# Kernel tuning notes

Measured on AMD Instinct MI355X. Metric: run time of the kernel, lower is better.

The kernel has to match this reference:

```python
import jax, jax.numpy as jnp
import numpy as np

# ---- SLAYER neuron / simulation params (network.yaml equivalents) ----
THETA = 10.0       # spiking threshold
TAU_SR = 10.0      # synaptic (PSP) alpha-kernel time constant
TAU_REF = 1.0      # refractory alpha-kernel time constant
SCALE_REF = 2.0
TS = 1.0           # simulation step
T_SAMPLE = 350     # number of timesteps

B, NIN, NHID, NOUT = 32, 2312, 512, 10


def _alpha_kernel(tau, mult=1.0, eps=0.01):
    # mirrors slayer._calculateAlphaKernel truncation rule
    ks = []
    for t in np.arange(0.0, T_SAMPLE, TS):
        v = mult * t / tau * np.exp(1.0 - t / tau)
        if abs(v) < eps and t > tau:
            break
        ks.append(v)
    return jnp.asarray(np.asarray(ks, dtype=np.float32))

SRM_KERNEL = _alpha_kernel(TAU_SR)                        # truncated PSP kernel
D_REF = float(np.exp(-TS / TAU_REF))                      # geometric decay of refractory alpha kernel
C_REF = float(-SCALE_REF * THETA * np.e * TS / TAU_REF)   # refKernel[j] = C_REF * j * D_REF**j


def psp(x):
    # causal temporal conv with the SRM alpha kernel, scaled by Ts. x: (B, C, T)
    b, c, t = x.shape
    k = SRM_KERNEL.shape[0]
    out = jax.lax.conv_general_dilated(
        x.reshape(b * c, 1, t), SRM_KERNEL[::-1].reshape(1, 1, k),
        window_strides=(1,), padding=[(k - 1, 0)])
    return (out * TS).reshape(b, c, t)


def spike(u_psp):
    # Sequential thresholding with FULL refractory recurrence: a spike at time s
    # adds refKernel[n-s] = C_REF*(n-s)*D_REF**(n-s) to all future potentials.
    # The alpha kernel is realized EXACTLY by a 2-state linear recurrence (x, y):
    #   x[n] = sum_s spk[s] * d^(n-s),  y[n] = sum_s spk[s] * (n-s) * d^(n-s)
    def step(carry, p_t):
        x, y = carry
        y = D_REF * (y + x)
        u = p_t + C_REF * y           # membrane potential after refractory response
        spk = (u >= THETA).astype(p_t.dtype)
        x = D_REF * x + spk
        return (x, y), spk / TS       # SLAYER emits spikes of magnitude 1/Ts
    b, c, _ = u_psp.shape
    init = (jnp.zeros((b, c), u_psp.dtype), jnp.zeros((b, c), u_psp.dtype))
    _, s = jax.lax.scan(step, init, jnp.moveaxis(u_psp, -1, 0))
    return jnp.moveaxis(s, 0, -1)


def setup_inputs() -> dict:
    key = jax.random.key(0)
    k1, k2, k3 = jax.random.split(key, 3)
    spikeInput = (jax.random.uniform(k1, (B, NIN, T_SAMPLE)) < 0.03).astype(jnp.float32) / TS
    W1 = jax.random.normal(k2, (NHID, NIN), jnp.float32) * 0.05
    W2 = jax.random.normal(k3, (NOUT, NHID), jnp.float32) * 0.5
    return {"spikeInput": spikeInput, "W1": W1, "W2": W2}


def reference(spikeInput, W1, W2):
    # fc (1x1x1 conv == per-timestep matmul) -> psp -> spike, twice
    s1 = spike(psp(jnp.einsum('oi,bit->bot', W1, spikeInput)))
    s2 = spike(psp(jnp.einsum('oi,bit->bot', W2, s1)))
    return s2
```

## Files before the change

kernel.cpp:

```cpp
#include <hip/hip_runtime.h>
#include <hip/hip_bf16.h>
#include <math.h>

#define B_    32
#define NIN_  2312
#define NHID_ 512
#define NOUT_ 10
#define T_    350
#define KLEN  77
#define MW    40
#define NIB   37
#define NTB   6
#define MAXA2 320

__global__ __launch_bounds__(256) void w1t_k(const float* __restrict__ W,
                                             float* __restrict__ WT) {
  __shared__ float tile[32][33];
  int i0 = blockIdx.x * 32, o0 = blockIdx.y * 32;
  int tx = threadIdx.x, tyb = threadIdx.y;
#pragma unroll
  for (int s = 0; s < 4; ++s) {
    int ty = tyb + s * 8;
    int o = o0 + ty, i = i0 + tx;
    if (i < NIN_) tile[ty][tx] = W[(size_t)o * NIN_ + i];
  }
  __syncthreads();
#pragma unroll
  for (int s = 0; s < 4; ++s) {
    int ty = tyb + s * 8;
    int i = i0 + ty, o = o0 + tx;
    if (i < NIN_) WT[(size_t)i * NHID_ + o] = tile[tx][ty];
  }
}

__global__ __launch_bounds__(256) void inmask_k(const float* __restrict__ X,
                                                unsigned long long* __restrict__ msk) {
  __shared__ unsigned short bits[64][4];
  int blk = blockIdx.x;
  int tb = blk % NTB;
  int rem = blk / NTB;
  int iblk = rem % NIB;
  int b = rem / NIB;
  int tid = threadIdx.x;
  int r = tid >> 2, c = tid & 3;
  int i = iblk * 64 + r;
  int tbase = tb * 64 + c * 16;
  bool rowok = (i < NIN_);
  const float2* rp = (const float2*)(X + ((size_t)b * NIN_ + (rowok ? i : 0)) * T_ + tbase);
  unsigned m = 0;
#define LD_(Q)                                                                 \
  {                                                                            \
    float2 vq = (rowok && (tbase + 2 * (Q) + 1) < T_) ? rp[Q]                  \
                                                      : make_float2(0.f, 0.f); \
    m |= (vq.x != 0.f ? 1u : 0u) << (2 * (Q));                                 \
    m |= (vq.y != 0.f ? 1u : 0u) << (2 * (Q) + 1);                             \
  }
  LD_(0) LD_(1) LD_(2) LD_(3) LD_(4) LD_(5) LD_(6) LD_(7)
#undef LD_
  bits[r][c] = (unsigned short)m;
  __syncthreads();
  int w = tid >> 6, lane = tid & 63;
  unsigned bm = bits[lane][w];
  unsigned long long* mrow = msk + ((size_t)b * T_ + (size_t)tb * 64 + w * 16) * MW + iblk;
  int tb16 = tb * 64 + w * 16;
#define BAL_(P)                                                                \
  {                                                                            \
    unsigned long long bw_ = __ballot(((bm >> (P)) & 1u) != 0u);               \
    if ((tb16 + (P)) < T_ && lane == (P)) mrow[(size_t)(P) * MW] = bw_;        \
  }
  BAL_(0)  BAL_(1)  BAL_(2)  BAL_(3)  BAL_(4)  BAL_(5)  BAL_(6)  BAL_(7)
  BAL_(8)  BAL_(9)  BAL_(10) BAL_(11) BAL_(12) BAL_(13) BAL_(14) BAL_(15)
#undef BAL_
}

__global__ __launch_bounds__(64) void accum1_k(const unsigned long long* __restrict__ msk,
                                               const float* __restrict__ WT,
                                               float* __restrict__ Z1) {
  __shared__ unsigned short list[MAXA2];
  int id = blockIdx.x;
  int bt = id >> 1, oc = id & 1;
  int lane = threadIdx.x;
  unsigned long long wm = (lane < NIB) ? msk[(size_t)bt * MW + lane] : 0ull;
  int pc = __popcll(wm);
  int pre = pc;
#pragma unroll
  for (int d = 1; d < 64; d <<= 1) {
    int o = __shfl_up(pre, d);
    if (lane >= d) pre += o;
  }
  int base = pre - pc;
  int n = __shfl(pre, 63);
  while (wm) {
    int j = __builtin_ctzll(wm);
    if (base < MAXA2) list[base] = (unsigned short)(lane * 64 + j);
    ++base;
    wm &= wm - 1;
  }
  __syncthreads();
  if (n > MAXA2) n = MAXA2;
  const float4* wbase = (const float4*)WT + (size_t)oc * 64 + lane;
  float4 acc = make_float4(0.f, 0.f, 0.f, 0.f);
#pragma unroll 8
  for (int j = 0; j < n; ++j) {
    float4 v = wbase[(size_t)list[j] * (NHID_ / 4)];
    acc.x += v.x;
    acc.y += v.y;
    acc.z += v.z;
    acc.w += v.w;
  }
  ((float4*)(Z1 + (size_t)bt * NHID_))[(size_t)oc * 64 + lane] = acc;
}

__global__ __launch_bounds__(64) void scan1_k(const float* __restrict__ Z1,
                                              unsigned long long* __restrict__ mask) {
  int lane = threadIdx.x;
  int b = blockIdx.x >> 3, g = blockIdx.x & 7;
  int h = g * 64 + lane;
  const double dp   = exp(-0.1);
  const double Ap   = exp(1.0) / 10.0;
  const double D77  = exp(-7.7);
  const float  Dref = (float)exp(-1.0);
  const float  Cref = (float)(-20.0 * exp(1.0));
  double Xc = 0.0, Yc = 0.0, Xd = 0.0, Yd = 0.0;
  float xr = 0.f, yr = 0.f;
  const float* zb = Z1 + (size_t)b * T_ * NHID_ + h;
  unsigned long long* mb = mask + (size_t)b * T_ * 8 + g;
  for (int t0 = 0; t0 < T_; t0 += 16) {
    float z[16], zd[16];
#pragma unroll
    for (int k = 0; k < 16; ++k) {
      int t = t0 + k;
      z[k]  = (t < T_) ? zb[(size_t)t * NHID_] : 0.f;
      zd[k] = (t >= KLEN && t < T_) ? zb[(size_t)(t - KLEN) * NHID_] : 0.f;
    }
#pragma unroll
    for (int k = 0; k < 16; ++k) {
      int t = t0 + k;
      if (t >= T_) break;
      Yc = dp * (Yc + Xc); Xc = dp * Xc + (double)z[k];
      Yd = dp * (Yd + Xd); Xd = dp * Xd + (double)zd[k];
      float p = (float)(Ap * (Yc - D77 * (Yd + 77.0 * Xd)));
      yr = Dref * (yr + xr);
      float u = p + Cref * yr;
      float s = (u >= 10.0f) ? 1.0f : 0.0f;
      xr = Dref * xr + s;
      unsigned long long bw = __ballot(u >= 10.0f);
      if (lane == 0) mb[(size_t)t * 8] = bw;
    }
  }
}

__global__ __launch_bounds__(256) void z2_k(const unsigned long long* __restrict__ mask,
                                            const float* __restrict__ W2,
                                            float* __restrict__ Z2) {
  int wave = blockIdx.x * 4 + (threadIdx.x >> 6);
  int lane = threadIdx.x & 63;
  if (wave >= B_ * T_) return;
  int b = wave / T_, t = wave - b * T_;
  const unsigned long long* m = mask + (size_t)wave * 8;
  if (lane < NOUT_) {
    const float* wr = W2 + (size_t)lane * NHID_;
    float acc = 0.f;
#pragma unroll
    for (int w = 0; w < 8; ++w) {
      unsigned long long mm = m[w];
      while (mm) {
        int j = __builtin_ctzll(mm);
        mm &= mm - 1;
        acc += wr[w * 64 + j];
      }
    }
    Z2[((size_t)b * NOUT_ + lane) * T_ + t] = acc;
  }
}

__global__ __launch_bounds__(64) void scan2_k(const float* __restrict__ Z2,
                                              float* __restrict__ out) {
  int n = blockIdx.x * 64 + threadIdx.x;
  if (n >= B_ * NOUT_) return;
  const double dp   = exp(-0.1);
  const double Ap   = exp(1.0) / 10.0;
  const double D77  = exp(-7.7);
  const float  Dref = (float)exp(-1.0);
  const float  Cref = (float)(-20.0 * exp(1.0));
  double Xc = 0.0, Yc = 0.0, Xd = 0.0, Yd = 0.0;
  float xr = 0.f, yr = 0.f;
  const float* row = Z2 + (size_t)n * T_;
  float* orow = out + (size_t)n * T_;
  for (int t0 = 0; t0 < T_; t0 += 16) {
    float z[16], zd[16];
#pragma unroll
    for (int k = 0; k < 16; ++k) {
      int t = t0 + k;
      z[k]  = (t < T_) ? row[t] : 0.f;
      zd[k] = (t >= KLEN && t < T_) ? row[t - KLEN] : 0.f;
    }
#pragma unroll
    for (int k = 0; k < 16; ++k) {
      int t = t0 + k;
      if (t >= T_) break;
      Yc = dp * (Yc + Xc); Xc = dp * Xc + (double)z[k];
      Yd = dp * (Yd + Xd); Xd = dp * Xd + (double)zd[k];
      float p = (float)(Ap * (Yc - D77 * (Yd + 77.0 * Xd)));
      yr = Dref * (yr + xr);
      float u = p + Cref * yr;
      float s = (u >= 10.0f) ? 1.0f : 0.0f;
      xr = Dref * xr + s;
      orow[t] = s;
    }
  }
}

extern "C" void kernel_launch(void* const* d_in, const int* in_sizes, int n_in,
                              void* d_out, int out_size, void* d_ws, size_t ws_size,
                              hipStream_t stream) {
  const float* X  = (const float*)d_in[0];
  const float* W1 = (const float*)d_in[1];
  const float* W2 = (const float*)d_in[2];
  float* out = (float*)d_out;

  char* ws = (char*)d_ws;
  size_t off = 0;
  float* W1T = (float*)(ws + off);                 off += (size_t)NIN_ * NHID_ * 4;
  unsigned long long* msk = (unsigned long long*)(ws + off); off += (size_t)B_ * T_ * MW * 8;
  float* Z1 = (float*)(ws + off);                  off += (size_t)B_ * T_ * NHID_ * 4;
  unsigned long long* mask = (unsigned long long*)(ws + off); off += (size_t)B_ * T_ * 8 * 8;
  float* Z2 = (float*)(ws + off);                  off += (size_t)B_ * NOUT_ * T_ * 4;
  if (off > ws_size) return;

  w1t_k<<<dim3((NIN_ + 31) / 32, NHID_ / 32), dim3(32, 8), 0, stream>>>(W1, W1T);
  inmask_k<<<B_ * NIB * NTB, 256, 0, stream>>>(X, msk);
  accum1_k<<<B_ * T_ * 2, 64, 0, stream>>>(msk, W1T, Z1);
  scan1_k<<<B_ * 8, 64, 0, stream>>>(Z1, mask);
  z2_k<<<(B_ * T_ + 3) / 4, 256, 0, stream>>>(mask, W2, Z2);
  scan2_k<<<(B_ * NOUT_ + 63) / 64, 64, 0, stream>>>(Z2, out);
}
```

Baseline: 385.8 us.

## Restructure input bitmask kernel for coalesced row loads and loop over time blocks

Result: faster. 354.7 us (-8.1%).

```diff
diff --git a/kernel.cpp b/kernel.cpp
--- a/kernel.cpp
+++ b/kernel.cpp
@@ -35,42 +35,53 @@
 
 __global__ __launch_bounds__(256) void inmask_k(const float* __restrict__ X,
                                                 unsigned long long* __restrict__ msk) {
-  __shared__ unsigned short bits[64][4];
+  __shared__ unsigned evens[64], odds[64];
   int blk = blockIdx.x;
-  int tb = blk % NTB;
-  int rem = blk / NTB;
-  int iblk = rem % NIB;
-  int b = rem / NIB;
+  int iblk = blk % NIB;
+  int b = blk / NIB;
   int tid = threadIdx.x;
-  int r = tid >> 2, c = tid & 3;
-  int i = iblk * 64 + r;
-  int tbase = tb * 64 + c * 16;
-  bool rowok = (i < NIN_);
-  const float2* rp = (const float2*)(X + ((size_t)b * NIN_ + (rowok ? i : 0)) * T_ + tbase);
-  unsigned m = 0;
-#define LD_(Q)                                                                 \
+  int w = tid >> 6, lane = tid & 63;
+  int rhalf = lane >> 5;
+  int c2 = lane & 31;
+  const float* base = X + ((size_t)b * NIN_ + (size_t)iblk * 64) * T_;
+  for (int tb = 0; tb < NTB; ++tb) {
+    int tbase = tb * 64;
+#define PH1_(Q)                                                                \
   {                                                                            \
-    float2 vq = (rowok && (tbase + 2 * (Q) + 1) < T_) ? rp[Q]                  \
-                                                      : make_float2(0.f, 0.f); \
-    m |= (vq.x != 0.f ? 1u : 0u) << (2 * (Q));                                 \
-    m |= (vq.y != 0.f ? 1u : 0u) << (2 * (Q) + 1);                             \
-  }
-  LD_(0) LD_(1) LD_(2) LD_(3) LD_(4) LD_(5) LD_(6) LD_(7)
-#undef LD_
-  bits[r][c] = (unsigned short)m;
-  __syncthreads();
-  int w = tid >> 6, lane = tid & 63;
-  unsigned bm = bits[lane][w];
-  unsigned long long* mrow = msk + ((size_t)b * T_ + (size_t)tb * 64 + w * 16) * MW + iblk;
-  int tb16 = tb * 64 + w * 16;
+    int row = 16 * w + 2 * (Q) + rhalf;                                        \
+    bool ok = (iblk * 64 + row) < NIN_ && (tbase + 2 * c2) < T_;               \
+    const float* rp = base + (size_t)row * T_ + tbase + 2 * c2;                \
+    float2 v = ok ? *(const float2*)rp : make_float2(0.f, 0.f);                \
+    unsigned long long be = __ballot(v.x != 0.f);                              \
+    unsigned long long bo = __ballot(v.y != 0.f);                              \
+    if (lane == 0) {                                                           \
+      evens[16 * w + 2 * (Q)] = (unsigned)be;                                  \
+      odds[16 * w + 2 * (Q)] = (unsigned)bo;                                   \
+    }                                                                          \
+    if (lane == 1) {                                                           \
+      evens[16 * w + 2 * (Q) + 1] = (unsigned)(be >> 32);                      \
+      odds[16 * w + 2 * (Q) + 1] = (unsigned)(bo >> 32);                       \
+    }                                                                          \
+  }
+    PH1_(0) PH1_(1) PH1_(2) PH1_(3) PH1_(4) PH1_(5) PH1_(6) PH1_(7)
+#undef PH1_
+    __syncthreads();
+    unsigned ev = evens[lane], od = odds[lane];
+    unsigned long long* mrow =
+        msk + ((size_t)b * T_ + tbase + w * 16) * MW + iblk;
 #define BAL_(P)                                                                \
   {                                                                            \
-    unsigned long long bw_ = __ballot(((bm >> (P)) & 1u) != 0u);               \
-    if ((tb16 + (P)) < T_ && lane == (P)) mrow[(size_t)(P) * MW] = bw_;        \
-  }
-  BAL_(0)  BAL_(1)  BAL_(2)  BAL_(3)  BAL_(4)  BAL_(5)  BAL_(6)  BAL_(7)
-  BAL_(8)  BAL_(9)  BAL_(10) BAL_(11) BAL_(12) BAL_(13) BAL_(14) BAL_(15)
+    unsigned sel = ((P) & 1) ? od : ev;                                        \
+    unsigned long long bw_ =                                                   \
+        __ballot(((sel >> (w * 8 + ((P) >> 1))) & 1u) != 0u);                  \
+    if (lane == (P) && (tbase + w * 16 + (P)) < T_)                            \
+      mrow[(size_t)(P) * MW] = bw_;                                            \
+  }
+    BAL_(0)  BAL_(1)  BAL_(2)  BAL_(3)  BAL_(4)  BAL_(5)  BAL_(6)  BAL_(7)
+    BAL_(8)  BAL_(9)  BAL_(10) BAL_(11) BAL_(12) BAL_(13) BAL_(14) BAL_(15)
 #undef BAL_
+    __syncthreads();
+  }
 }
 
 __global__ __launch_bounds__(64) void accum1_k(const unsigned long long* __restrict__ msk,
@@ -100,7 +111,7 @@
   if (n > MAXA2) n = MAXA2;
   const float4* wbase = (const float4*)WT + (size_t)oc * 64 + lane;
   float4 acc = make_float4(0.f, 0.f, 0.f, 0.f);
-#pragma unroll 8
+#pragma unroll 16
   for (int j = 0; j < n; ++j) {
     float4 v = wbase[(size_t)list[j] * (NHID_ / 4)];
     acc.x += v.x;
@@ -229,7 +240,7 @@
   if (off > ws_size) return;
 
   w1t_k<<<dim3((NIN_ + 31) / 32, NHID_ / 32), dim3(32, 8), 0, stream>>>(W1, W1T);
-  inmask_k<<<B_ * NIB * NTB, 256, 0, stream>>>(X, msk);
+  inmask_k<<<B_ * NIB, 256, 0, stream>>>(X, msk);
   accum1_k<<<B_ * T_ * 2, 64, 0, stream>>>(msk, W1T, Z1);
   scan1_k<<<B_ * 8, 64, 0, stream>>>(Z1, mask);
   z2_k<<<(B_ * T_ + 3) / 4, 256, 0, stream>>>(mask, W2, Z2);
```
